# Optimization experiments

Measured on AMD Instinct MI355X. Metric: run time of the kernel, lower is better.

The kernel has to match this reference:

```python
import jax, jax.numpy as jnp
import numpy as np

B, S, E, H, D = 4, 2048, 512, 8, 64
NEG = 1e13  # module uses -1e13, not -inf


def setup_inputs() -> dict:
    key = jax.random.key(0)
    ks = jax.random.split(key, 10)
    x = jax.random.normal(ks[0], (B, S, E), dtype=jnp.float32)
    padding_pos = jax.random.randint(ks[1], (B, S), 0, 2, dtype=jnp.int64)
    std = 0.01
    # weights stored [in, out]; torch Linear init: normal(0, 0.01) weights, default bias
    Wq = jax.random.normal(ks[2], (E, H * D), dtype=jnp.float32) * std
    Wk = jax.random.normal(ks[3], (E, H * D), dtype=jnp.float32) * std
    Wv = jax.random.normal(ks[4], (E, H * D), dtype=jnp.float32) * std
    Wo = jax.random.normal(ks[5], (H * D, E), dtype=jnp.float32) * std
    bq = jax.random.uniform(ks[6], (H * D,), dtype=jnp.float32, minval=-1, maxval=1) / np.sqrt(E)
    bk = jax.random.uniform(ks[7], (H * D,), dtype=jnp.float32, minval=-1, maxval=1) / np.sqrt(E)
    bv = jax.random.uniform(ks[8], (H * D,), dtype=jnp.float32, minval=-1, maxval=1) / np.sqrt(E)
    bo = jax.random.uniform(ks[9], (E,), dtype=jnp.float32, minval=-1, maxval=1) / np.sqrt(H * D)
    return {"x": x, "padding_pos": padding_pos, "Wq": Wq, "bq": bq, "Wk": Wk,
            "bk": bk, "Wv": Wv, "bv": bv, "Wo": Wo, "bo": bo}


def reference(x, padding_pos, Wq, bq, Wk, bk, Wv, bv, Wo, bo):
    b = x.shape[0]
    q = (x @ Wq + bq).reshape(b, S, H, D).transpose(0, 2, 1, 3)  # [B,H,S,D]
    k = (x @ Wk + bk).reshape(b, S, H, D).transpose(0, 2, 1, 3)
    v = (x @ Wv + bv).reshape(b, S, H, D).transpose(0, 2, 1, 3)
    att = jnp.einsum('bhqd,bhkd->bhqk', q, k) / jnp.sqrt(jnp.float32(D))
    pad = (padding_pos == 1)  # [B,S]
    # mask key columns and query rows (module masks both via broadcast fills)
    mask = pad[:, None, None, :] | pad[:, None, :, None]  # [B,1,S,S]
    att = jnp.where(mask, -NEG, att)
    att = jax.nn.softmax(att, axis=-1)
    out = jnp.einsum('bhqk,bhkd->bhqd', att, v)
    out = out.transpose(0, 2, 1, 3).reshape(b, S, H * D)
    return out @ Wo + bo
```

## Files before the change

kernel.cpp:

```cpp
#include <hip/hip_runtime.h>
#include <hip/hip_bf16.h>
#include <math.h>

#define Bb 4
#define Ss 2048
#define Ee 512
#define Hh 8
#define Dd 64
#define HD 512
#define Mm (Bb*Ss)
#define RPB 1536
#define QT2 12

using bf16x8 = __attribute__((ext_vector_type(8))) short;
using f32x4  = __attribute__((ext_vector_type(4))) float;
using f32x16 = __attribute__((ext_vector_type(16))) float;

typedef __attribute__((address_space(1))) const unsigned int gu32;
typedef __attribute__((address_space(3))) unsigned int lu32;
__device__ inline void glds16(const void* g, void* l) {
    __builtin_amdgcn_global_load_lds((gu32*)g, (lu32*)l, 16, 0, 0);
}

__device__ inline unsigned short f2bf(float f) {
    unsigned int u = __float_as_uint(f);
    unsigned int r = (u + 0x7fffu + ((u >> 16) & 1u)) >> 16;
    return (unsigned short)r;
}
__device__ inline float bf2f(unsigned short u) {
    return __uint_as_float((unsigned int)u << 16);
}
__device__ inline unsigned int cvtpk(float a, float b) {
    float2 t; t.x = a; t.y = b;
    union { __hip_bfloat162 h; unsigned int u; } z;
    z.h = __float22bfloat162_rn(t);
    return z.u;
}

__global__ __launch_bounds__(256) void prep2(
    const float* __restrict__ x, const int* __restrict__ pad,
    const float* __restrict__ Wq, const float* __restrict__ Wk,
    const float* __restrict__ Wv, const float* __restrict__ Wo,
    unsigned short* __restrict__ Wt, unsigned short* __restrict__ xc,
    float* __restrict__ xpart, int* __restrict__ idx, int* __restrict__ cnt)
{
    __shared__ union ShMem {
        float T[64][68];
        struct { int sc[256]; int rk[64]; float sm[4][512]; } g;
    } sh;
    const int bi = blockIdx.x, tid = threadIdx.x;

    if (bi < 256) {
        const int w = bi >> 6;
        const float* W = (w == 0) ? Wq : (w == 1) ? Wk : (w == 2) ? Wv : Wo;
        const int tk0 = ((bi >> 3) & 7) * 64, tn0 = (bi & 7) * 64;
        #pragma unroll
        for (int l = 0; l < 4; ++l) {
            int fi = tid + l * 256;
            int r = fi >> 4, c4 = (fi & 15) * 4;
            *(float4*)&sh.T[r][c4] = *(const float4*)(W + (size_t)(tk0 + r) * Ee + tn0 + c4);
        }
        __syncthreads();
        #pragma unroll
        for (int l = 0; l < 4; ++l) {
            int fi = tid + l * 256;
            int r2 = fi >> 4, c4 = (fi & 15) * 4;
            uint2 o;
            o.x = cvtpk(sh.T[c4 + 0][r2], sh.T[c4 + 1][r2]);
            o.y = cvtpk(sh.T[c4 + 2][r2], sh.T[c4 + 3][r2]);
            *(uint2*)(Wt + (size_t)w * 262144 + (size_t)(tn0 + r2) * Ee + tk0 + c4) = o;
        }
        return;
    }

    const int gb = bi - 256;
    const int b = gb >> 5, i = gb & 31;

    int loc[8], c = 0;
    #pragma unroll
    for (int j = 0; j < 8; ++j) {
        loc[j] = pad[b * Ss + tid * 8 + j];
        c += (loc[j] == 0);
    }
    sh.g.sc[tid] = c;
    __syncthreads();
    for (int s = 1; s < 256; s <<= 1) {
        int v = (tid >= s) ? sh.g.sc[tid - s] : 0;
        __syncthreads();
        sh.g.sc[tid] += v;
        __syncthreads();
    }
    if (tid >= i * 8 && tid < i * 8 + 8) {
        int off = sh.g.sc[tid] - c;
        int lbase = (tid - i * 8) * 8;
        #pragma unroll
        for (int j = 0; j < 8; ++j) {
            if (loc[j] == 0) {
                idx[b * Ss + off] = tid * 8 + j;
                sh.g.rk[lbase + j] = off;
                ++off;
            } else sh.g.rk[lbase + j] = -1;
        }
    }
    if (i == 31 && tid == 255) cnt[b] = sh.g.sc[255];
    __syncthreads();

    const int c8 = (tid & 63) * 8, grp = tid >> 6;
    float a8[8] = {};
    for (int it = 0; it < 16; ++it) {
        int lr = grp * 16 + it;
        int s = i * 64 + lr;
        const float* pr = x + ((size_t)b * Ss + s) * Ee + c8;
        float4 f0 = *(const float4*)pr;
        float4 f1 = *(const float4*)(pr + 4);
        a8[0] += f0.x; a8[1] += f0.y; a8[2] += f0.z; a8[3] += f0.w;
        a8[4] += f1.x; a8[5] += f1.y; a8[6] += f1.z; a8[7] += f1.w;
        int rkk = sh.g.rk[lr];
        if (rkk >= 0) {
            uint4 v;
            v.x = cvtpk(f0.x, f0.y); v.y = cvtpk(f0.z, f0.w);
            v.z = cvtpk(f1.x, f1.y); v.w = cvtpk(f1.z, f1.w);
            *(uint4*)(xc + ((size_t)b * RPB + rkk) * Ee + c8) = v;
        }
    }
    #pragma unroll
    for (int j = 0; j < 8; ++j) sh.g.sm[grp][c8 + j] = a8[j];
    __syncthreads();
    int c0 = tid * 2;
    float s0 = sh.g.sm[0][c0] + sh.g.sm[1][c0] + sh.g.sm[2][c0] + sh.g.sm[3][c0];
    float s1 = sh.g.sm[0][c0 + 1] + sh.g.sm[1][c0 + 1] + sh.g.sm[2][c0 + 1] + sh.g.sm[3][c0 + 1];
    float2 o; o.x = s0; o.y = s1;
    *(float2*)(xpart + (size_t)(b * 32 + i) * Ee + c0) = o;
}

__global__ __launch_bounds__(256) void gemm_qkvt(
    const unsigned short* __restrict__ xc, const unsigned short* __restrict__ Wt,
    const float* __restrict__ bq, const float* __restrict__ bk, const float* __restrict__ bv,
    const int* __restrict__ cnt, const float* __restrict__ xpart,
    unsigned short* __restrict__ qo, unsigned short* __restrict__ ko,
    unsigned short* __restrict__ vt, float* __restrict__ vmw)
{
    const int z = blockIdx.z;
    const int bx = blockIdx.x;
    const int b = bx / 48, t = bx - b * 48;
    const int at = (z < 2) ? (t >> 2) : (t & 3);
    const int bt = (z < 2) ? (t & 3) : (t >> 2);
    const int cntb = cnt[b];
    const int tid = threadIdx.x, lane = tid & 63, wv = tid >> 6;
    const int quad = lane >> 4, l15 = lane & 15;
    const int wm = (wv >> 1) * 64, wn = (wv & 1) * 64;
    const int sw = (l15 >> 1) & 3;

    __shared__ unsigned short As0[128][32], Bs0[128][32];
    __shared__ unsigned short As1[128][32], Bs1[128][32];

    if (z == 2 && bt == 11) {
        float* xm = (float*)&As0[0][0];
        for (int kk = tid; kk < 512; kk += 256) {
            float s = 0.f;
            #pragma unroll
            for (int p = 0; p < 32; ++p) s += xpart[(size_t)(b * 32 + p) * Ee + kk];
            xm[kk] = s;
        }
        __syncthreads();
        int col = at * 128 + (tid >> 1);
        int kh = (tid & 1) * 256;
        const unsigned short* wrow = Wt + (size_t)2 * 262144 + (size_t)col * Ee + kh;
        float s = 0.f;
        #pragma unroll 8
        for (int kk = 0; kk < 256; ++kk) s += xm[kh + kk] * bf2f(wrow[kk]);
        s += __shfl_xor(s, 1);
        if ((tid & 1) == 0) vmw[(size_t)b * HD + col] = s * (1.0f / 2048.0f) + bv[col];
        return;
    }

    const int xcTile = (z < 2) ? at : bt;
    if (xcTile * 128 >= cntb) return;

    const unsigned short *Ap, *Bp;
    if (z < 2) {
        Ap = xc + ((size_t)b * RPB + at * 128) * Ee;
        Bp = Wt + (size_t)z * 262144 + (size_t)bt * 128 * Ee;
    } else {
        Ap = Wt + (size_t)2 * 262144 + (size_t)at * 128 * Ee;
        Bp = xc + ((size_t)b * RPB + bt * 128) * Ee;
    }

    f32x4 acc[4][4] = {};

    auto stage = [&](unsigned short (&A)[128][32], unsigned short (&B)[128][32], int k0) {
        #pragma unroll
        for (int l = 0; l < 2; ++l) {
            int id = tid + l * 256;
            int r = id >> 2, c = id & 3;
            int cg = (c ^ ((r >> 1) & 3)) * 8;
            glds16(Ap + (size_t)r * Ee + k0 + cg, &A[r][c * 8]);
            glds16(Bp + (size_t)r * Ee + k0 + cg, &B[r][c * 8]);
        }
    };
    auto compute = [&](const unsigned short (&A)[128][32], const unsigned short (&B)[128][32]) {
        bf16x8 af[4], bfr[4];
        #pragma unroll
        for (int ms = 0; ms < 4; ++ms) af[ms] = *(const bf16x8*)&A[wm + ms * 16 + l15][(quad ^ sw) * 8];
        #pragma unroll
        for (int ns = 0; ns < 4; ++ns) bfr[ns] = *(const bf16x8*)&B[wn + ns * 16 + l15][(quad ^ sw) * 8];
        #pragma unroll
        for (int ms = 0; ms < 4; ++ms)
            #pragma unroll
            for (int ns = 0; ns < 4; ++ns)
                acc[ms][ns] = __builtin_amdgcn_mfma_f32_16x16x32_bf16(af[ms], bfr[ns], acc[ms][ns], 0, 0, 0);
    };

    stage(As0, Bs0, 0);
    for (int ki = 0; ki < 16; ki += 2) {
        __syncthreads();
        if (ki + 1 < 16) stage(As1, Bs1, (ki + 1) * 32);
        compute(As0, Bs0);
        __syncthreads();
        if (ki + 2 < 16) stage(As0, Bs0, (ki + 2) * 32);
        compute(As1, Bs1);
    }

    if (z < 2) {
        const float* bias = z ? bk : bq;
        unsigned short* dst = z ? ko : qo;
        #pragma unroll
        for (int ns = 0; ns < 4; ++ns) {
            int col = bt * 128 + wn + ns * 16 + l15;
            float bb = bias[col];
            #pragma unroll
            for (int ms = 0; ms < 4; ++ms) {
                #pragma unroll
                for (int r = 0; r < 4; ++r) {
                    int m = at * 128 + wm + ms * 16 + quad * 4 + r;
                    float val = acc[ms][ns][r] + bb;
                    if (z == 0) val *= 0.18033688f;
                    dst[((size_t)b * RPB + m) * HD + col] = f2bf(val);
                }
            }
        }
    } else {
        #pragma unroll
        for (int ms = 0; ms < 4; ++ms) {
            #pragma unroll
            for (int r = 0; r < 4; ++r) {
                int dg = at * 128 + wm + ms * 16 + quad * 4 + r;
                float bb = bv[dg];
                #pragma unroll
                for (int ns = 0; ns < 4; ++ns) {
                    int col = bt * 128 + wn + ns * 16 + l15;
                    vt[((size_t)b * HD + dg) * RPB + col] = f2bf(acc[ms][ns][r] + bb);
                }
            }
        }
    }
}

__global__ __launch_bounds__(256, 2) void attn(
    const unsigned short* __restrict__ qc, const unsigned short* __restrict__ kc,
    const unsigned short* __restrict__ vtc, const int* __restrict__ cnt,
    unsigned short* __restrict__ pO, float* __restrict__ pL,
    const float* __restrict__ vmw, const unsigned short* __restrict__ Wt,
    const float* __restrict__ bo, float* __restrict__ opad)
{
    __shared__ unsigned short Ks[2][64][64], Vs[2][64][64];

    const int tid = threadIdx.x, wv = tid >> 6, lane = tid & 63;
    const int l31 = lane & 31, hlf = lane >> 5;
    const int bh = blockIdx.x, b = bh >> 3, hd = bh & 7;
    const int qt = blockIdx.y, half = blockIdx.z;

    if (qt >= QT2) {
        if (half || bh >= 8) return;
        const int b2 = bh >> 1, seg = bh & 1;
        float* vm = (float*)&Ks[0][0][0];
        for (int t = tid; t < 512; t += 256) vm[t] = vmw[(size_t)b2 * HD + t];
        __syncthreads();
        int ccc = seg * 256 + tid;
        const unsigned short* wrow = Wt + (size_t)3 * 262144 + (size_t)ccc * HD;
        float s = 0.f;
        #pragma unroll 8
        for (int k = 0; k < 512; ++k) s += vm[k] * bf2f(wrow[k]);
        opad[(size_t)b2 * Ee + ccc] = s + bo[ccc];
        return;
    }

    const int cntb = cnt[b];
    if (qt * 128 >= cntb) return;

    const int tot = (cntb + 63) >> 6;
    const int hsplit = (tot + 1) >> 1;
    const int kstart = half ? hsplit : 0;
    const int kend = half ? tot : hsplit;

    const int qrow = qt * 128 + wv * 32 + l31;
    const unsigned short* qp = qc + ((size_t)b * RPB + qrow) * HD + hd * Dd + hlf * 8;
    bf16x8 qf0 = *(const bf16x8*)(qp);
    bf16x8 qf1 = *(const bf16x8*)(qp + 16);
    bf16x8 qf2 = *(const bf16x8*)(qp + 32);
    bf16x8 qf3 = *(const bf16x8*)(qp + 48);

    const unsigned short* kcb = kc + (size_t)b * RPB * HD + hd * Dd;
    const unsigned short* vtb = vtc + ((size_t)b * HD + hd * Dd) * RPB;

    const int srow = tid >> 3, scp = tid & 7;
    auto STAGE = [&](int bufi, int kt_) {
        const int k0_ = kt_ * 64;
        const int sc = (scp ^ (srow & 7)) * 8;
        glds16(kcb + (size_t)(k0_ + srow) * HD + sc, &Ks[bufi][srow][scp * 8]);
        glds16(vtb + (size_t)srow * RPB + k0_ + sc, &Vs[bufi][srow][scp * 8]);
        glds16(kcb + (size_t)(k0_ + srow + 32) * HD + sc, &Ks[bufi][srow + 32][scp * 8]);
        glds16(vtb + (size_t)(srow + 32) * RPB + k0_ + sc, &Vs[bufi][srow + 32][scp * 8]);
    };

    float li = 0.f;
    f32x16 oa0 = {0,0,0,0,0,0,0,0,0,0,0,0,0,0,0,0};
    f32x16 oa1 = {0,0,0,0,0,0,0,0,0,0,0,0,0,0,0,0};
    const int rs = l31 & 7;

    int cur = 0;
    STAGE(0, kstart);
    for (int kt = kstart; kt < kend; ++kt) {
        asm volatile("" ::: "memory");
        __builtin_amdgcn_s_barrier();
        if (kt + 1 < kend) {
            STAGE(cur ^ 1, kt + 1);
            asm volatile("s_waitcnt vmcnt(4)" ::: "memory");
        } else {
            asm volatile("s_waitcnt vmcnt(0)" ::: "memory");
        }
        __builtin_amdgcn_s_barrier();
        asm volatile("" ::: "memory");

        const int k0 = kt * 64;

        f32x16 sa0 = {0,0,0,0,0,0,0,0,0,0,0,0,0,0,0,0};
        f32x16 sa1 = {0,0,0,0,0,0,0,0,0,0,0,0,0,0,0,0};
        __builtin_amdgcn_s_setprio(1);
        {
            bf16x8 kf;
            #define QKSTEP(dg, qf) \
                kf = *(const bf16x8*)&Ks[cur][l31][(((dg)*2 + hlf) ^ rs) * 8]; \
                sa0 = __builtin_amdgcn_mfma_f32_32x32x16_bf16(kf, qf, sa0, 0, 0, 0); \
                kf = *(const bf16x8*)&Ks[cur][32 + l31][(((dg)*2 + hlf) ^ rs) * 8]; \
                sa1 = __builtin_amdgcn_mfma_f32_32x32x16_bf16(kf, qf, sa1, 0, 0, 0);
            QKSTEP(0, qf0) QKSTEP(1, qf1) QKSTEP(2, qf2) QKSTEP(3, qf3)
            #undef QKSTEP
        }
        __builtin_amdgcn_s_setprio(0);

        if (kt == tot - 1 && (cntb & 63)) {
            #pragma unroll
            for (int r = 0; r < 16; ++r) {
                int kl = k0 + (r & 3) + 8 * (r >> 2) + 4 * hlf;
                if (kl >= cntb) sa0[r] = -1e30f;
                if (kl + 32 >= cntb) sa1[r] = -1e30f;
            }
        }
        float p0[16], p1[16];
        #pragma unroll
        for (int r = 0; r < 16; ++r) { p0[r] = exp2f(sa0[r]); li += p0[r]; }
        #pragma unroll
        for (int r = 0; r < 16; ++r) { p1[r] = exp2f(sa1[r]); li += p1[r]; }

        union U8 { unsigned int u[4]; bf16x8 v8; };
        U8 pf0, pf1, pf2, pf3;
        {
            unsigned int w00 = cvtpk(p0[0],  p0[1]),  w01 = cvtpk(p0[2],  p0[3]);
            unsigned int w10 = cvtpk(p0[4],  p0[5]),  w11 = cvtpk(p0[6],  p0[7]);
            unsigned int w20 = cvtpk(p0[8],  p0[9]),  w21 = cvtpk(p0[10], p0[11]);
            unsigned int w30 = cvtpk(p0[12], p0[13]), w31 = cvtpk(p0[14], p0[15]);
            asm volatile("v_permlane32_swap_b32 %0, %1" : "+v"(w00), "+v"(w10));
            asm volatile("v_permlane32_swap_b32 %0, %1" : "+v"(w01), "+v"(w11));
            asm volatile("v_permlane32_swap_b32 %0, %1" : "+v"(w20), "+v"(w30));
            asm volatile("v_permlane32_swap_b32 %0, %1" : "+v"(w21), "+v"(w31));
            pf0.u[0] = w00; pf0.u[1] = w01; pf0.u[2] = w10; pf0.u[3] = w11;
            pf1.u[0] = w20; pf1.u[1] = w21; pf1.u[2] = w30; pf1.u[3] = w31;
        }
        {
            unsigned int w00 = cvtpk(p1[0],  p1[1]),  w01 = cvtpk(p1[2],  p1[3]);
            unsigned int w10 = cvtpk(p1[4],  p1[5]),  w11 = cvtpk(p1[6],  p1[7]);
            unsigned int w20 = cvtpk(p1[8],  p1[9]),  w21 = cvtpk(p1[10], p1[11]);
            unsigned int w30 = cvtpk(p1[12], p1[13]), w31 = cvtpk(p1[14], p1[15]);
            asm volatile("v_permlane32_swap_b32 %0, %1" : "+v"(w00), "+v"(w10));
            asm volatile("v_permlane32_swap_b32 %0, %1" : "+v"(w01), "+v"(w11));
            asm volatile("v_permlane32_swap_b32 %0, %1" : "+v"(w20), "+v"(w30));
            asm volatile("v_permlane32_swap_b32 %0, %1" : "+v"(w21), "+v"(w31));
            pf2.u[0] = w00; pf2.u[1] = w01; pf2.u[2] = w10; pf2.u[3] = w11;
            pf3.u[0] = w20; pf3.u[1] = w21; pf3.u[2] = w30; pf3.u[3] = w31;
        }

        __builtin_amdgcn_s_setprio(1);
        {
            bf16x8 vf;
            #define PVSTEP(kcc, pf) \
                vf = *(const bf16x8*)&Vs[cur][l31][(((kcc)*2 + hlf) ^ rs) * 8]; \
                oa0 = __builtin_amdgcn_mfma_f32_32x32x16_bf16(pf.v8, vf, oa0, 0, 0, 0); \
                vf = *(const bf16x8*)&Vs[cur][32 + l31][(((kcc)*2 + hlf) ^ rs) * 8]; \
                oa1 = __builtin_amdgcn_mfma_f32_32x32x16_bf16(pf.v8, vf, oa1, 0, 0, 0);
            PVSTEP(0, pf0) PVSTEP(1, pf1) PVSTEP(2, pf2) PVSTEP(3, pf3)
            #undef PVSTEP
        }
        __builtin_amdgcn_s_setprio(0);

        cur ^= 1;
    }

    li += __shfl_xor(li, 32);
    const size_t pbase = (((size_t)bh * QT2 + qt) * 2 + half) * (size_t)8192;
    const size_t lbase = (((size_t)bh * QT2 + qt) * 2 + half) * (size_t)128;
    if (hlf == 0) pL[lbase + wv * 32 + l31] = li;
    #pragma unroll
    for (int r = 0; r < 16; ++r) {
        int ql = (r & 3) + 8 * (r >> 2) + 4 * hlf;
        size_t rb = pbase + (size_t)(wv * 32 + ql) * 64;
        pO[rb + l31]      = f2bf(oa0[r]);
        pO[rb + 32 + l31] = f2bf(oa1[r]);
    }
}

__global__ __launch_bounds__(256) void gemm_out(
    const unsigned short* __restrict__ pO, const float* __restrict__ pL,
    const unsigned short* __restrict__ Wt, const float* __restrict__ bo,
    const int* __restrict__ idx, const int* __restrict__ cnt,
    const int* __restrict__ pad, const float* __restrict__ out_pad,
    float* __restrict__ out)
{
    const int bx = blockIdx.x;
    const int tid = threadIdx.x;

    if (bx >= Bb * 48) {
        const int fb = bx - Bb * 48;
        const int b = fb >> 3, seg = fb & 7;
        const int c0 = tid * 2;
        float2 op = *(const float2*)(out_pad + (size_t)b * Ee + c0);
        for (int r = 0; r < 256; ++r) {
            int s = seg * 256 + r;
            if (pad[b * Ss + s])
                *(float2*)(out + ((size_t)b * Ss + s) * Ee + c0) = op;
        }
        return;
    }

    const int b = bx / 48, t = bx - b * 48;
    const int at = t >> 2, bt = t & 3;
    const int cntb = cnt[b];
    if (at * 128 >= cntb) return;

    const unsigned short* Wz = Wt + (size_t)3 * 262144;
    const int lane = tid & 63, wv = tid >> 6;
    const int quad = lane >> 4, l15 = lane & 15;
    const int wm = (wv >> 1) * 64, wn = (wv & 1) * 64;
    const int sw = (l15 >> 1) & 3;
    const unsigned short* Bp = Wz + (size_t)bt * 128 * HD;

    __shared__ unsigned short As0[128][32], Bs0[128][32];
    __shared__ unsigned short As1[128][32], Bs1[128][32];
    __shared__ float invSh[1024];

    #pragma unroll
    for (int l = 0; l < 4; ++l) {
        int ix = tid + l * 256;
        int h = ix >> 7, row = ix & 127;
        size_t lb = (((size_t)(b * 8 + h) * QT2 + at) * 2) * 128;
        float lsum = pL[lb + row] + pL[lb + 128 + row];
        invSh[ix] = (lsum > 0.f) ? 1.0f / lsum : 0.f;
    }
    __syncthreads();

    f32x4 acc[4][4] = {};

    auto stageA = [&](unsigned short (&A)[128][32], int k0) {
        #pragma unroll
        for (int l = 0; l < 2; ++l) {
            int id = tid + l * 256;
            int r = id >> 2, c = id & 3;
            int swr = (r >> 1) & 3;
            int h = k0 >> 6;
            int d0 = (k0 & 63) + c * 8;
            const size_t pb = (((size_t)((b * 8 + h) * QT2 + at) * 2)) * 8192 + (size_t)r * 64 + d0;
            union { uint4 q; unsigned short u[8]; } pa, pbh;
            pa.q  = *(const uint4*)(pO + pb);
            pbh.q = *(const uint4*)(pO + pb + 8192);
            float inv = invSh[h * 128 + r];
            uint4 o;
            o.x = cvtpk((bf2f(pa.u[0]) + bf2f(pbh.u[0])) * inv, (bf2f(pa.u[1]) + bf2f(pbh.u[1])) * inv);
            o.y = cvtpk((bf2f(pa.u[2]) + bf2f(pbh.u[2])) * inv, (bf2f(pa.u[3]) + bf2f(pbh.u[3])) * inv);
            o.z = cvtpk((bf2f(pa.u[4]) + bf2f(pbh.u[4])) * inv, (bf2f(pa.u[5]) + bf2f(pbh.u[5])) * inv);
            o.w = cvtpk((bf2f(pa.u[6]) + bf2f(pbh.u[6])) * inv, (bf2f(pa.u[7]) + bf2f(pbh.u[7])) * inv);
            *(uint4*)&A[r][(c ^ swr) * 8] = o;
        }
    };
    auto stageB = [&](unsigned short (&B)[128][32], int k0) {
        #pragma unroll
        for (int l = 0; l < 2; ++l) {
            int id = tid + l * 256;
            int r = id >> 2, c = id & 3;
            int cg = (c ^ ((r >> 1) & 3)) * 8;
            glds16(Bp + (size_t)r * HD + k0 + cg, &B[r][c * 8]);
        }
    };
    auto compute = [&](const unsigned short (&A)[128][32], const unsigned short (&B)[128][32]) {
        bf16x8 af[4], bfr[4];
        #pragma unroll
        for (int ms = 0; ms < 4; ++ms) af[ms] = *(const bf16x8*)&A[wm + ms * 16 + l15][(quad ^ sw) * 8];
        #pragma unroll
        for (int ns = 0; ns < 4; ++ns) bfr[ns] = *(const bf16x8*)&B[wn + ns * 16 + l15][(quad ^ sw) * 8];
        #pragma unroll
        for (int ms = 0; ms < 4; ++ms)
            #pragma unroll
            for (int ns = 0; ns < 4; ++ns)
                acc[ms][ns] = __builtin_amdgcn_mfma_f32_16x16x32_bf16(af[ms], bfr[ns], acc[ms][ns], 0, 0, 0);
    };

    stageA(As0, 0); stageB(Bs0, 0);
    for (int ki = 0; ki < 16; ki += 2) {
        __syncthreads();
        if (ki + 1 < 16) { stageA(As1, (ki + 1) * 32); stageB(Bs1, (ki + 1) * 32); }
        compute(As0, Bs0);
        __syncthreads();
        if (ki + 2 < 16) { stageA(As0, (ki + 2) * 32); stageB(Bs0, (ki + 2) * 32); }
        compute(As1, Bs1);
    }

    #pragma unroll
    for (int ns = 0; ns < 4; ++ns) {
        int col = bt * 128 + wn + ns * 16 + l15;
        float bb = bo[col];
        #pragma unroll
        for (int ms = 0; ms < 4; ++ms) {
            #pragma unroll
            for (int r = 0; r < 4; ++r) {
                int m = at * 128 + wm + ms * 16 + quad * 4 + r;
                if (m < cntb) {
                    int srow = idx[b * Ss + m];
                    out[((size_t)b * Ss + srow) * Ee + col] = acc[ms][ns][r] + bb;
                }
            }
        }
    }
}

extern "C" void kernel_launch(void* const* d_in, const int* in_sizes, int n_in,
                              void* d_out, int out_size, void* d_ws, size_t ws_size,
                              hipStream_t stream) {
    const float* x   = (const float*)d_in[0];
    const int*   pad = (const int*)  d_in[1];
    const float* Wq  = (const float*)d_in[2];
    const float* bq  = (const float*)d_in[3];
    const float* Wk  = (const float*)d_in[4];
    const float* bk  = (const float*)d_in[5];
    const float* Wv  = (const float*)d_in[6];
    const float* bv  = (const float*)d_in[7];
    const float* Wo  = (const float*)d_in[8];
    const float* bo  = (const float*)d_in[9];
    float* out = (float*)d_out;

    const size_t csz = (size_t)Bb * RPB * HD;
    unsigned short* Wt  = (unsigned short*)d_ws;
    unsigned short* qc  = Wt + 1048576;
    unsigned short* kc  = qc + csz;
    unsigned short* vtc = kc + csz;
    unsigned short* xc  = vtc + csz;
    unsigned short* pO  = xc;
    unsigned short* tail = xc + 6291456;
    float* xpart = (float*)tail;
    int*   idxw  = (int*)(xpart + 128 * 512);
    int*   cntw  = idxw + Mm;
    float* vmw   = (float*)(cntw + 4);
    float* opad  = vmw + Bb * HD;
    float* pLw   = opad + Bb * Ee;

    prep2<<<384, 256, 0, stream>>>(x, pad, Wq, Wk, Wv, Wo, Wt, xc, xpart, idxw, cntw);

    dim3 g1(Bb * 48, 1, 3);
    gemm_qkvt<<<g1, 256, 0, stream>>>(xc, Wt, bq, bk, bv, cntw, xpart, qc, kc, vtc, vmw);

    dim3 g2(Bb * Hh, QT2 + 1, 2);
    attn<<<g2, 256, 0, stream>>>(qc, kc, vtc, cntw, pO, pLw, vmw, Wt, bo, opad);

    dim3 g3(Bb * 48 + 32, 1);
    gemm_out<<<g3, 256, 0, stream>>>(pO, pLw, Wt, bo, idxw, cntw, pad, opad, out);
}
```

Before: 160.0 us.

## Drop split-K attention partials; normalize in attn and load O directly in out GEMM

```diff
diff --git a/kernel.cpp b/kernel.cpp
--- a/kernel.cpp
+++ b/kernel.cpp
@@ -259,7 +259,7 @@
 __global__ __launch_bounds__(256, 2) void attn(
     const unsigned short* __restrict__ qc, const unsigned short* __restrict__ kc,
     const unsigned short* __restrict__ vtc, const int* __restrict__ cnt,
-    unsigned short* __restrict__ pO, float* __restrict__ pL,
+    unsigned short* __restrict__ Oc,
     const float* __restrict__ vmw, const unsigned short* __restrict__ Wt,
     const float* __restrict__ bo, float* __restrict__ opad)
 {
@@ -268,10 +268,10 @@
     const int tid = threadIdx.x, wv = tid >> 6, lane = tid & 63;
     const int l31 = lane & 31, hlf = lane >> 5;
     const int bh = blockIdx.x, b = bh >> 3, hd = bh & 7;
-    const int qt = blockIdx.y, half = blockIdx.z;
+    const int qt = blockIdx.y;
 
     if (qt >= QT2) {
-        if (half || bh >= 8) return;
+        if (bh >= 8) return;
         const int b2 = bh >> 1, seg = bh & 1;
         float* vm = (float*)&Ks[0][0][0];
         for (int t = tid; t < 512; t += 256) vm[t] = vmw[(size_t)b2 * HD + t];
@@ -289,9 +289,6 @@
     if (qt * 128 >= cntb) return;
 
     const int tot = (cntb + 63) >> 6;
-    const int hsplit = (tot + 1) >> 1;
-    const int kstart = half ? hsplit : 0;
-    const int kend = half ? tot : hsplit;
 
     const int qrow = qt * 128 + wv * 32 + l31;
     const unsigned short* qp = qc + ((size_t)b * RPB + qrow) * HD + hd * Dd + hlf * 8;
@@ -319,11 +316,11 @@
     const int rs = l31 & 7;
 
     int cur = 0;
-    STAGE(0, kstart);
-    for (int kt = kstart; kt < kend; ++kt) {
+    STAGE(0, 0);
+    for (int kt = 0; kt < tot; ++kt) {
         asm volatile("" ::: "memory");
         __builtin_amdgcn_s_barrier();
-        if (kt + 1 < kend) {
+        if (kt + 1 < tot) {
             STAGE(cur ^ 1, kt + 1);
             asm volatile("s_waitcnt vmcnt(4)" ::: "memory");
         } else {
@@ -407,20 +404,23 @@
     }
 
     li += __shfl_xor(li, 32);
-    const size_t pbase = (((size_t)bh * QT2 + qt) * 2 + half) * (size_t)8192;
-    const size_t lbase = (((size_t)bh * QT2 + qt) * 2 + half) * (size_t)128;
-    if (hlf == 0) pL[lbase + wv * 32 + l31] = li;
+    float* Ls = (float*)&Ks[0][0][0];
+    __syncthreads();
+    if (hlf == 0) Ls[wv * 32 + l31] = (li > 0.f) ? 1.0f / li : 0.f;
+    __syncthreads();
+
+    unsigned short* oc = Oc + ((size_t)b * RPB + qt * 128 + wv * 32) * HD + hd * Dd;
     #pragma unroll
     for (int r = 0; r < 16; ++r) {
         int ql = (r & 3) + 8 * (r >> 2) + 4 * hlf;
-        size_t rb = pbase + (size_t)(wv * 32 + ql) * 64;
-        pO[rb + l31]      = f2bf(oa0[r]);
-        pO[rb + 32 + l31] = f2bf(oa1[r]);
+        float inv = Ls[wv * 32 + ql];
+        oc[(size_t)ql * HD + l31]      = f2bf(oa0[r] * inv);
+        oc[(size_t)ql * HD + 32 + l31] = f2bf(oa1[r] * inv);
     }
 }
 
 __global__ __launch_bounds__(256) void gemm_out(
-    const unsigned short* __restrict__ pO, const float* __restrict__ pL,
+    const unsigned short* __restrict__ Oc,
     const unsigned short* __restrict__ Wt, const float* __restrict__ bo,
     const int* __restrict__ idx, const int* __restrict__ cnt,
     const int* __restrict__ pad, const float* __restrict__ out_pad,
@@ -452,51 +452,21 @@
     const int quad = lane >> 4, l15 = lane & 15;
     const int wm = (wv >> 1) * 64, wn = (wv & 1) * 64;
     const int sw = (l15 >> 1) & 3;
+    const unsigned short* Ap = Oc + ((size_t)b * RPB + at * 128) * HD;
     const unsigned short* Bp = Wz + (size_t)bt * 128 * HD;
 
     __shared__ unsigned short As0[128][32], Bs0[128][32];
     __shared__ unsigned short As1[128][32], Bs1[128][32];
-    __shared__ float invSh[1024];
-
-    #pragma unroll
-    for (int l = 0; l < 4; ++l) {
-        int ix = tid + l * 256;
-        int h = ix >> 7, row = ix & 127;
-        size_t lb = (((size_t)(b * 8 + h) * QT2 + at) * 2) * 128;
-        float lsum = pL[lb + row] + pL[lb + 128 + row];
-        invSh[ix] = (lsum > 0.f) ? 1.0f / lsum : 0.f;
-    }
-    __syncthreads();
 
     f32x4 acc[4][4] = {};
 
-    auto stageA = [&](unsigned short (&A)[128][32], int k0) {
-        #pragma unroll
-        for (int l = 0; l < 2; ++l) {
-            int id = tid + l * 256;
-            int r = id >> 2, c = id & 3;
-            int swr = (r >> 1) & 3;
-            int h = k0 >> 6;
-            int d0 = (k0 & 63) + c * 8;
-            const size_t pb = (((size_t)((b * 8 + h) * QT2 + at) * 2)) * 8192 + (size_t)r * 64 + d0;
-            union { uint4 q; unsigned short u[8]; } pa, pbh;
-            pa.q  = *(const uint4*)(pO + pb);
-            pbh.q = *(const uint4*)(pO + pb + 8192);
-            float inv = invSh[h * 128 + r];
-            uint4 o;
-            o.x = cvtpk((bf2f(pa.u[0]) + bf2f(pbh.u[0])) * inv, (bf2f(pa.u[1]) + bf2f(pbh.u[1])) * inv);
-            o.y = cvtpk((bf2f(pa.u[2]) + bf2f(pbh.u[2])) * inv, (bf2f(pa.u[3]) + bf2f(pbh.u[3])) * inv);
-            o.z = cvtpk((bf2f(pa.u[4]) + bf2f(pbh.u[4])) * inv, (bf2f(pa.u[5]) + bf2f(pbh.u[5])) * inv);
-            o.w = cvtpk((bf2f(pa.u[6]) + bf2f(pbh.u[6])) * inv, (bf2f(pa.u[7]) + bf2f(pbh.u[7])) * inv);
-            *(uint4*)&A[r][(c ^ swr) * 8] = o;
-        }
-    };
-    auto stageB = [&](unsigned short (&B)[128][32], int k0) {
+    auto stage = [&](unsigned short (&A)[128][32], unsigned short (&B)[128][32], int k0) {
         #pragma unroll
         for (int l = 0; l < 2; ++l) {
             int id = tid + l * 256;
             int r = id >> 2, c = id & 3;
             int cg = (c ^ ((r >> 1) & 3)) * 8;
+            glds16(Ap + (size_t)r * HD + k0 + cg, &A[r][c * 8]);
             glds16(Bp + (size_t)r * HD + k0 + cg, &B[r][c * 8]);
         }
     };
@@ -513,13 +483,13 @@
                 acc[ms][ns] = __builtin_amdgcn_mfma_f32_16x16x32_bf16(af[ms], bfr[ns], acc[ms][ns], 0, 0, 0);
     };
 
-    stageA(As0, 0); stageB(Bs0, 0);
+    stage(As0, Bs0, 0);
     for (int ki = 0; ki < 16; ki += 2) {
         __syncthreads();
-        if (ki + 1 < 16) { stageA(As1, (ki + 1) * 32); stageB(Bs1, (ki + 1) * 32); }
+        if (ki + 1 < 16) stage(As1, Bs1, (ki + 1) * 32);
         compute(As0, Bs0);
         __syncthreads();
-        if (ki + 2 < 16) { stageA(As0, (ki + 2) * 32); stageB(Bs0, (ki + 2) * 32); }
+        if (ki + 2 < 16) stage(As0, Bs0, (ki + 2) * 32);
         compute(As1, Bs1);
     }
 
@@ -562,23 +532,22 @@
     unsigned short* kc  = qc + csz;
     unsigned short* vtc = kc + csz;
     unsigned short* xc  = vtc + csz;
-    unsigned short* pO  = xc;
+    unsigned short* Oc  = xc;
     unsigned short* tail = xc + 6291456;
     float* xpart = (float*)tail;
     int*   idxw  = (int*)(xpart + 128 * 512);
     int*   cntw  = idxw + Mm;
     float* vmw   = (float*)(cntw + 4);
     float* opad  = vmw + Bb * HD;
-    float* pLw   = opad + Bb * Ee;
 
     prep2<<<384, 256, 0, stream>>>(x, pad, Wq, Wk, Wv, Wo, Wt, xc, xpart, idxw, cntw);
 
     dim3 g1(Bb * 48, 1, 3);
     gemm_qkvt<<<g1, 256, 0, stream>>>(xc, Wt, bq, bk, bv, cntw, xpart, qc, kc, vtc, vmw);
 
-    dim3 g2(Bb * Hh, QT2 + 1, 2);
-    attn<<<g2, 256, 0, stream>>>(qc, kc, vtc, cntw, pO, pLw, vmw, Wt, bo, opad);
+    dim3 g2(Bb * Hh, QT2 + 1, 1);
+    attn<<<g2, 256, 0, stream>>>(qc, kc, vtc, cntw, Oc, vmw, Wt, bo, opad);
 
     dim3 g3(Bb * 48 + 32, 1);
-    gemm_out<<<g3, 256, 0, stream>>>(pO, pLw, Wt, bo, idxw, cntw, pad, opad, out);
-}
+    gemm_out<<<g3, 256, 0, stream>>>(Oc, Wt, bo, idxw, cntw, pad, opad, out);
+}
```

After: 162.2 us. No clear change (+1.4%).
